# Optimization experiments

Hardware: AMD Instinct MI355X
Metric: run time of the kernel (lower is better)

## Reference

```python
import jax, jax.numpy as jnp
import numpy as np

F_FACETS = 400000
TEX_PER = 4            # textures per facet (counts sum must equal total textures)
T_TEX = F_FACETS * TEX_PER
C_IN = 64
C_OUT = 64
L = 2
N_BASIS = (L + 1) ** 2  # 9
BN_EPS = 1e-3


def setup_inputs() -> dict:
    key = jax.random.key(0)
    k1, k2, k3 = jax.random.split(key, 3)
    input_texture = jax.random.normal(k1, (T_TEX, C_IN), jnp.float32)
    bary_coeff = jax.random.uniform(k2, (T_TEX, N_BASIS), jnp.float32)
    # per-facet texture counts; constant 4 so counts sum exactly to T_TEX
    num_texture = jnp.full((F_FACETS,), TEX_PER, dtype=jnp.int32)
    # xavier_normal_ on [O, I, K]: fan_in = I*K, fan_out = ... torch uses fan_in=I*K? For 3D it treats dim1*rest.
    std = float(np.sqrt(2.0 / (C_IN * N_BASIS + C_OUT * N_BASIS)))
    weights = jax.random.normal(k3, (C_OUT, C_IN, N_BASIS), jnp.float32) * std
    biases = jnp.zeros((1, C_OUT), jnp.float32)
    gamma = jnp.ones((C_OUT,), jnp.float32)
    beta = jnp.zeros((C_OUT,), jnp.float32)
    return {
        "input_texture": input_texture,
        "bary_coeff": bary_coeff,
        "weights": weights,
        "biases": biases,
        "gamma": gamma,
        "beta": beta,
        "num_texture": num_texture,
    }


def reference(input_texture, bary_coeff, weights, biases, gamma, beta, num_texture):
    T = input_texture.shape[0]
    n_facets = num_texture.shape[0]
    n_basis = weights.shape[2]
    # per-texture contribution: contrib[t,o] = sum_{i,k} x[t,i] * W[o,i,k] * bary[t,k]
    # loop over small fixed basis count (9) to avoid a [T, I, K] intermediate
    contrib = jnp.zeros((T, weights.shape[0]), dtype=input_texture.dtype)
    for k in range(n_basis):
        contrib = contrib + (input_texture @ weights[:, :, k].T) * bary_coeff[:, k:k + 1]
    # scatter-sum per facet (ragged groups given by num_texture), then average
    seg_ids = jnp.repeat(jnp.arange(n_facets), num_texture, total_repeat_length=T)
    facet_sum = jax.ops.segment_sum(contrib, seg_ids, num_segments=n_facets)
    out = facet_sum / num_texture[:, None].astype(facet_sum.dtype)
    # bias + ReLU
    out = jax.nn.relu(out + biases)
    # BatchNorm1d in training mode: batch stats (biased variance), eps=1e-3
    mu = jnp.mean(out, axis=0)
    var = jnp.mean(jnp.square(out - mu), axis=0)
    out = (out - mu) * jax.lax.rsqrt(var + BN_EPS) * gamma + beta
    return out
```

## Files before the change

kernel.cpp:

```cpp
#include <hip/hip_runtime.h>


typedef _Float16 half8  __attribute__((ext_vector_type(8)));
typedef _Float16 h2     __attribute__((ext_vector_type(2)));
typedef __fp16   fp16x2 __attribute__((ext_vector_type(2)));
typedef float    f32x4  __attribute__((ext_vector_type(4)));

#define NGROUPS 100000
#define NPAIRS  50000
#define FFACETS 400000
#define GRID1   768
#define LDSP    9472

#define WAITV(N) asm volatile("s_waitcnt vmcnt(" #N ")" ::: "memory")
#define WAITL0() asm volatile("s_waitcnt lgkmcnt(0)" ::: "memory")
#define FENCE()  asm volatile("" ::: "memory")
#define SB0()    __builtin_amdgcn_sched_barrier(0)

union HF { h2 h[4]; half8 v; };

static __device__ __forceinline__ h2 pkrtz(float a, float b) {
    fp16x2 r = __builtin_amdgcn_cvt_pkrtz(a, b);
    return __builtin_bit_cast(h2, r);
}

static __device__ __forceinline__ void gload16(const void* g, void* l) {
    __builtin_amdgcn_global_load_lds((const __attribute__((address_space(1))) void*)g,
                                     (__attribute__((address_space(3))) void*)l, 16, 0, 0);
}

__global__ __launch_bounds__(256) void prep_kernel(const float* __restrict__ W,
                                                   _Float16* __restrict__ wswz,
                                                   float* __restrict__ stats) {
    int idx = blockIdx.x * 256 + threadIdx.x;
    if (idx < 36864) {
        int j    = idx & 7;
        int lane = (idx >> 3) & 63;
        int mt   = (idx >> 9) & 3;
        int c    = idx >> 11;
        int o    = mt * 16 + (lane & 15);
        int i    = (c & 1) * 32 + ((lane >> 4) << 3) + j;
        int kb   = c >> 1;
        wswz[idx] = (_Float16)W[(o * 64 + i) * 9 + kb];
    }
    if (idx < 128) stats[idx] = 0.0f;
}

__global__ __launch_bounds__(256, 3) void pass1_kernel(
    const float* __restrict__ X, const float* __restrict__ BARY,
    const _Float16* __restrict__ WSWZ, const float* __restrict__ BIAS,
    const int* __restrict__ NTEX, float* __restrict__ OUT,
    float* __restrict__ stats) {

    __shared__ __align__(16) char lds[2][LDSP];
    __shared__ float sl_s[64];
    __shared__ float sl_s2[64];

    const int tid  = threadIdx.x;
    const int wave = tid >> 6;
    const int lane = tid & 63;
    const int col  = lane & 15;
    const int quad = lane >> 4;

    half8 wf[18];
#pragma unroll
    for (int c = 0; c < 18; ++c)
        wf[c] = *(const half8*)(WSWZ + ((size_t)(c * 4 + wave) * 64 + lane) * 8);

    const f32x4 biasv = *(const f32x4*)(BIAS + wave * 16 + quad * 4);

    const int pphys  = (wave << 10) + (lane << 4);
    const int xsoff  = pphys ^ (((pphys >> 8) & 7) << 4);
    const char* Xb   = (const char*)X;
    const char* BAb  = (const char*)BARY;
    const char* NTb  = (const char*)NTEX;

    const int m    = (col & 7) << 4;
    const int a00  = (col << 8) + ((quad << 5) ^ m);
    const int a10  = (col << 8) + (((quad << 5) | 16) ^ m);
    const int bco  = 8192 + col * 36;
    const int nco  = 9344 + ((col >> 2) << 2);

    float sacc[4]  = {0.f, 0.f, 0.f, 0.f};
    float s2acc[4] = {0.f, 0.f, 0.f, 0.f};

    const int b = blockIdx.x;
    const int n = (NPAIRS - 1 - b) / GRID1 + 1;

    auto STAGE = [&](int p, int u) {
        const char* xs = Xb + (size_t)u * 8192;
        gload16(xs + xsoff,        &lds[p][pphys]);
        gload16(xs + 4096 + xsoff, &lds[p][4096 + pphys]);
        gload16(BAb + (size_t)u * 1152 + lane * 16, &lds[p][8192 + lane * 16]);
        if (lane < 8) gload16(BAb + (size_t)u * 1152 + 1024 + lane * 16, &lds[p][9216 + lane * 16]);
        if (lane < 2) gload16(NTb + (size_t)u * 32 + lane * 16,          &lds[p][9344 + lane * 16]);
    };

    auto EPI = [&](f32x4 acc, float rc, int f) {
        f32x4 vv;
#pragma unroll
        for (int r = 0; r < 4; ++r) {
            float s = acc[r];
            s += __shfl_xor(s, 1);
            s += __shfl_xor(s, 2);
            s = s * rc + biasv[r];
            s = s > 0.f ? s : 0.f;
            vv[r] = s;
            sacc[r]  += s;
            s2acc[r] += s * s;
        }
        if ((col & 3) == 0)
            *(f32x4*)(OUT + (size_t)f * 64 + wave * 16 + quad * 4) = vv;
    };

    auto ITER = [&](int p, int u, int upre, bool do_stage) {
        __builtin_amdgcn_s_barrier();
        FENCE();
        const char* L = lds[p];
        f32x4 r0[4], r1[4];
        r0[0] = *(const f32x4*)(L + a00);
        r0[1] = *(const f32x4*)(L + a10);
        r0[2] = *(const f32x4*)(L + a00 + 128);
        r0[3] = *(const f32x4*)(L + a10 + 128);
        r1[0] = *(const f32x4*)(L + 4096 + a00);
        r1[1] = *(const f32x4*)(L + 4096 + a10);
        r1[2] = *(const f32x4*)(L + 4096 + a00 + 128);
        r1[3] = *(const f32x4*)(L + 4096 + a10 + 128);
        float bF0[9], bF1[9];
#pragma unroll
        for (int k = 0; k < 9; ++k) bF0[k] = *(const float*)(L + bco + k * 4);
#pragma unroll
        for (int k = 0; k < 9; ++k) bF1[k] = *(const float*)(L + bco + 576 + k * 4);
        const int nt0 = *(const int*)(L + nco);
        const int nt1 = *(const int*)(L + nco + 16);

        h2 xh0[8], xh1[8], bh0[9], bh1[9];
        xh0[0] = pkrtz(r0[0][0], r0[0][1]);  xh0[1] = pkrtz(r0[0][2], r0[0][3]);
        xh0[2] = pkrtz(r0[1][0], r0[1][1]);  xh0[3] = pkrtz(r0[1][2], r0[1][3]);
        xh0[4] = pkrtz(r0[2][0], r0[2][1]);  xh0[5] = pkrtz(r0[2][2], r0[2][3]);
        xh0[6] = pkrtz(r0[3][0], r0[3][1]);  xh0[7] = pkrtz(r0[3][2], r0[3][3]);
        xh1[0] = pkrtz(r1[0][0], r1[0][1]);  xh1[1] = pkrtz(r1[0][2], r1[0][3]);
        xh1[2] = pkrtz(r1[1][0], r1[1][1]);  xh1[3] = pkrtz(r1[1][2], r1[1][3]);
        xh1[4] = pkrtz(r1[2][0], r1[2][1]);  xh1[5] = pkrtz(r1[2][2], r1[2][3]);
        xh1[6] = pkrtz(r1[3][0], r1[3][1]);  xh1[7] = pkrtz(r1[3][2], r1[3][3]);
#pragma unroll
        for (int k = 0; k < 9; ++k) { bh0[k] = pkrtz(bF0[k], bF0[k]); bh1[k] = pkrtz(bF1[k], bF1[k]); }
        const float rc0 = __builtin_amdgcn_rcpf((float)nt0);
        const float rc1 = __builtin_amdgcn_rcpf((float)nt1);

        WAITL0();
        SB0();
        __builtin_amdgcn_s_barrier();
        FENCE();
        if (do_stage) STAGE(p, upre);
        FENCE();

        f32x4 accA = {0.f, 0.f, 0.f, 0.f};
        f32x4 accB = {0.f, 0.f, 0.f, 0.f};
        __builtin_amdgcn_s_setprio(1);
#pragma unroll
        for (int c = 0; c < 18; ++c) {
            const int hh = (c & 1) * 4;
            const h2 bkA = bh0[c >> 1];
            const h2 bkB = bh1[c >> 1];
            HF fa, fb;
            fa.h[0] = xh0[hh + 0] * bkA;  fa.h[1] = xh0[hh + 1] * bkA;
            fa.h[2] = xh0[hh + 2] * bkA;  fa.h[3] = xh0[hh + 3] * bkA;
            accA = __builtin_amdgcn_mfma_f32_16x16x32_f16(wf[c], fa.v, accA, 0, 0, 0);
            fb.h[0] = xh1[hh + 0] * bkB;  fb.h[1] = xh1[hh + 1] * bkB;
            fb.h[2] = xh1[hh + 2] * bkB;  fb.h[3] = xh1[hh + 3] * bkB;
            accB = __builtin_amdgcn_mfma_f32_16x16x32_f16(wf[c], fb.v, accB, 0, 0, 0);
        }
        __builtin_amdgcn_s_setprio(0);

        const int f0 = u * 8 + (col >> 2);
        EPI(accA, rc0, f0);
        EPI(accB, rc1, f0 + 4);
    };

    STAGE(0, b);
    STAGE(1, b + GRID1);
    WAITV(5); ITER(0, b,         b + 2 * GRID1, true);
    WAITV(7); ITER(1, b + GRID1, b + 3 * GRID1, true);
    int t = 2;
    for (; t < n - 2; ++t) {
        WAITV(9);
        ITER(t & 1, b + t * GRID1, b + (t + 2) * GRID1, true);
    }
    WAITV(9); ITER(t & 1, b + t * GRID1, 0, false); ++t;
    WAITV(4); ITER(t & 1, b + t * GRID1, 0, false);

#pragma unroll
    for (int r = 0; r < 4; ++r) {
        float s = sacc[r], s2 = s2acc[r];
        s  += __shfl_xor(s, 1);  s  += __shfl_xor(s, 2);
        s  += __shfl_xor(s, 4);  s  += __shfl_xor(s, 8);
        s2 += __shfl_xor(s2, 1); s2 += __shfl_xor(s2, 2);
        s2 += __shfl_xor(s2, 4); s2 += __shfl_xor(s2, 8);
        if (col == 0) {
            sl_s [wave * 16 + quad * 4 + r] = s  * 0.25f;
            sl_s2[wave * 16 + quad * 4 + r] = s2 * 0.25f;
        }
    }
    __syncthreads();
    if (tid < 64)        atomicAdd(&stats[tid],      sl_s [tid]);
    else if (tid < 128)  atomicAdd(&stats[tid],      sl_s2[tid - 64]);
}

__global__ __launch_bounds__(256) void pass3_kernel(float* __restrict__ OUT,
    const float* __restrict__ stats, const float* __restrict__ gamma,
    const float* __restrict__ beta) {
    const int tid = threadIdx.x;
    const size_t l = (size_t)blockIdx.x * 256 + tid;
    const int c0 = ((int)l & 15) * 4;
    float mu[4], sc[4], be[4];
    const float invF = 1.0f / (float)FFACETS;
#pragma unroll
    for (int u = 0; u < 4; ++u) {
        int ch = c0 + u;
        float m  = stats[ch] * invF;
        float va = stats[64 + ch] * invF - m * m;
        mu[u] = m;
        sc[u] = rsqrtf(va + 1e-3f) * gamma[ch];
        be[u] = beta[ch];
    }
    const size_t n4 = (size_t)FFACETS * 16;
    for (size_t i = l; i < n4; i += (size_t)gridDim.x * 256) {
        f32x4 v = ((f32x4*)OUT)[i];
#pragma unroll
        for (int u = 0; u < 4; ++u)
            v[u] = (v[u] - mu[u]) * sc[u] + be[u];
        ((f32x4*)OUT)[i] = v;
    }
}

extern "C" void kernel_launch(void* const* d_in, const int* in_sizes, int n_in,
                              void* d_out, int out_size, void* d_ws, size_t ws_size,
                              hipStream_t stream) {
    const float* X     = (const float*)d_in[0];
    const float* BARY  = (const float*)d_in[1];
    const float* W     = (const float*)d_in[2];
    const float* BIAS  = (const float*)d_in[3];
    const float* GAMMA = (const float*)d_in[4];
    const float* BETA  = (const float*)d_in[5];
    const int*   NTEX  = (const int*)d_in[6];
    float* OUT = (float*)d_out;

    _Float16* wswz = (_Float16*)d_ws;
    float* stats   = (float*)((char*)d_ws + 73728);

    prep_kernel<<<144, 256, 0, stream>>>(W, wswz, stats);
    pass1_kernel<<<GRID1, 256, 0, stream>>>(X, BARY, wswz, BIAS, NTEX, OUT, stats);
    pass3_kernel<<<2048, 256, 0, stream>>>(OUT, stats, GAMMA, BETA);
}
```

Measured before the change: 674.4 us.

## Fuse BatchNorm pass into main kernel via grid barrier and restructure MFMA basis accumulation

Removes the separate normalization kernel by adding a software grid-wide barrier (atomic counter plus spin) at the end of pass1, after which every block normalizes its own facet pairs in place. The MFMA loop now feeds fp16 inputs directly with separate accumulators per basis, and applies the barycentric weights in fp32 afterwards. This avoids the fp16 multiplies and the extra fp16 rounding of the input, at the cost of more accumulator registers. The grid drops to 512 blocks with occupancy 2 so that all blocks can be co-resident for the barrier, which risks deadlock if they are not.

```diff
diff --git a/kernel.cpp b/kernel.cpp
--- a/kernel.cpp
+++ b/kernel.cpp
@@ -5,11 +5,12 @@
 typedef _Float16 h2     __attribute__((ext_vector_type(2)));
 typedef __fp16   fp16x2 __attribute__((ext_vector_type(2)));
 typedef float    f32x4  __attribute__((ext_vector_type(4)));
+typedef float    f32x2  __attribute__((ext_vector_type(2)));
 
 #define NGROUPS 100000
 #define NPAIRS  50000
 #define FFACETS 400000
-#define GRID1   768
+#define GRID1   512
 #define LDSP    9472
 
 #define WAITV(N) asm volatile("s_waitcnt vmcnt(" #N ")" ::: "memory")
@@ -17,7 +18,7 @@
 #define FENCE()  asm volatile("" ::: "memory")
 #define SB0()    __builtin_amdgcn_sched_barrier(0)
 
-union HF { h2 h[4]; half8 v; };
+union H8 { h2 h[4]; half8 v; };
 
 static __device__ __forceinline__ h2 pkrtz(float a, float b) {
     fp16x2 r = __builtin_amdgcn_cvt_pkrtz(a, b);
@@ -43,14 +44,15 @@
         int kb   = c >> 1;
         wswz[idx] = (_Float16)W[(o * 64 + i) * 9 + kb];
     }
-    if (idx < 128) stats[idx] = 0.0f;
-}
-
-__global__ __launch_bounds__(256, 3) void pass1_kernel(
+    if (idx < 132) stats[idx] = 0.0f;
+}
+
+__global__ __launch_bounds__(256, 2) void pass1_kernel(
     const float* __restrict__ X, const float* __restrict__ BARY,
     const _Float16* __restrict__ WSWZ, const float* __restrict__ BIAS,
     const int* __restrict__ NTEX, float* __restrict__ OUT,
-    float* __restrict__ stats) {
+    float* __restrict__ stats, const float* __restrict__ GAMMA,
+    const float* __restrict__ BETA) {
 
     __shared__ __align__(16) char lds[2][LDSP];
     __shared__ float sl_s[64];
@@ -134,17 +136,15 @@
         const int nt0 = *(const int*)(L + nco);
         const int nt1 = *(const int*)(L + nco + 16);
 
-        h2 xh0[8], xh1[8], bh0[9], bh1[9];
-        xh0[0] = pkrtz(r0[0][0], r0[0][1]);  xh0[1] = pkrtz(r0[0][2], r0[0][3]);
-        xh0[2] = pkrtz(r0[1][0], r0[1][1]);  xh0[3] = pkrtz(r0[1][2], r0[1][3]);
-        xh0[4] = pkrtz(r0[2][0], r0[2][1]);  xh0[5] = pkrtz(r0[2][2], r0[2][3]);
-        xh0[6] = pkrtz(r0[3][0], r0[3][1]);  xh0[7] = pkrtz(r0[3][2], r0[3][3]);
-        xh1[0] = pkrtz(r1[0][0], r1[0][1]);  xh1[1] = pkrtz(r1[0][2], r1[0][3]);
-        xh1[2] = pkrtz(r1[1][0], r1[1][1]);  xh1[3] = pkrtz(r1[1][2], r1[1][3]);
-        xh1[4] = pkrtz(r1[2][0], r1[2][1]);  xh1[5] = pkrtz(r1[2][2], r1[2][3]);
-        xh1[6] = pkrtz(r1[3][0], r1[3][1]);  xh1[7] = pkrtz(r1[3][2], r1[3][3]);
-#pragma unroll
-        for (int k = 0; k < 9; ++k) { bh0[k] = pkrtz(bF0[k], bF0[k]); bh1[k] = pkrtz(bF1[k], bF1[k]); }
+        H8 xlo0, xhi0, xlo1, xhi1;
+        xlo0.h[0] = pkrtz(r0[0][0], r0[0][1]);  xlo0.h[1] = pkrtz(r0[0][2], r0[0][3]);
+        xlo0.h[2] = pkrtz(r0[1][0], r0[1][1]);  xlo0.h[3] = pkrtz(r0[1][2], r0[1][3]);
+        xhi0.h[0] = pkrtz(r0[2][0], r0[2][1]);  xhi0.h[1] = pkrtz(r0[2][2], r0[2][3]);
+        xhi0.h[2] = pkrtz(r0[3][0], r0[3][1]);  xhi0.h[3] = pkrtz(r0[3][2], r0[3][3]);
+        xlo1.h[0] = pkrtz(r1[0][0], r1[0][1]);  xlo1.h[1] = pkrtz(r1[0][2], r1[0][3]);
+        xlo1.h[2] = pkrtz(r1[1][0], r1[1][1]);  xlo1.h[3] = pkrtz(r1[1][2], r1[1][3]);
+        xhi1.h[0] = pkrtz(r1[2][0], r1[2][1]);  xhi1.h[1] = pkrtz(r1[2][2], r1[2][3]);
+        xhi1.h[2] = pkrtz(r1[3][0], r1[3][1]);  xhi1.h[3] = pkrtz(r1[3][2], r1[3][3]);
         const float rc0 = __builtin_amdgcn_rcpf((float)nt0);
         const float rc1 = __builtin_amdgcn_rcpf((float)nt1);
 
@@ -155,24 +155,31 @@
         if (do_stage) STAGE(p, upre);
         FENCE();
 
-        f32x4 accA = {0.f, 0.f, 0.f, 0.f};
-        f32x4 accB = {0.f, 0.f, 0.f, 0.f};
+        f32x4 acc0[9], acc1[9];
+#pragma unroll
+        for (int k = 0; k < 9; ++k) { acc0[k] = (f32x4){0,0,0,0}; acc1[k] = (f32x4){0,0,0,0}; }
         __builtin_amdgcn_s_setprio(1);
 #pragma unroll
-        for (int c = 0; c < 18; ++c) {
-            const int hh = (c & 1) * 4;
-            const h2 bkA = bh0[c >> 1];
-            const h2 bkB = bh1[c >> 1];
-            HF fa, fb;
-            fa.h[0] = xh0[hh + 0] * bkA;  fa.h[1] = xh0[hh + 1] * bkA;
-            fa.h[2] = xh0[hh + 2] * bkA;  fa.h[3] = xh0[hh + 3] * bkA;
-            accA = __builtin_amdgcn_mfma_f32_16x16x32_f16(wf[c], fa.v, accA, 0, 0, 0);
-            fb.h[0] = xh1[hh + 0] * bkB;  fb.h[1] = xh1[hh + 1] * bkB;
-            fb.h[2] = xh1[hh + 2] * bkB;  fb.h[3] = xh1[hh + 3] * bkB;
-            accB = __builtin_amdgcn_mfma_f32_16x16x32_f16(wf[c], fb.v, accB, 0, 0, 0);
+        for (int kb = 0; kb < 9; ++kb) {
+            acc0[kb] = __builtin_amdgcn_mfma_f32_16x16x32_f16(wf[2 * kb],     xlo0.v, acc0[kb], 0, 0, 0);
+            acc1[kb] = __builtin_amdgcn_mfma_f32_16x16x32_f16(wf[2 * kb],     xlo1.v, acc1[kb], 0, 0, 0);
+            acc0[kb] = __builtin_amdgcn_mfma_f32_16x16x32_f16(wf[2 * kb + 1], xhi0.v, acc0[kb], 0, 0, 0);
+            acc1[kb] = __builtin_amdgcn_mfma_f32_16x16x32_f16(wf[2 * kb + 1], xhi1.v, acc1[kb], 0, 0, 0);
         }
         __builtin_amdgcn_s_setprio(0);
 
+        f32x4 accA, accB;
+#pragma unroll
+        for (int r = 0; r < 4; ++r) {
+            float sA = bF0[0] * acc0[0][r];
+            float sB = bF1[0] * acc1[0][r];
+#pragma unroll
+            for (int k = 1; k < 9; ++k) {
+                sA = __builtin_fmaf(bF0[k], acc0[k][r], sA);
+                sB = __builtin_fmaf(bF1[k], acc1[k][r], sB);
+            }
+            accA[r] = sA; accB[r] = sB;
+        }
         const int f0 = u * 8 + (col >> 2);
         EPI(accA, rc0, f0);
         EPI(accB, rc1, f0 + 4);
@@ -205,32 +212,35 @@
     __syncthreads();
     if (tid < 64)        atomicAdd(&stats[tid],      sl_s [tid]);
     else if (tid < 128)  atomicAdd(&stats[tid],      sl_s2[tid - 64]);
-}
-
-__global__ __launch_bounds__(256) void pass3_kernel(float* __restrict__ OUT,
-    const float* __restrict__ stats, const float* __restrict__ gamma,
-    const float* __restrict__ beta) {
-    const int tid = threadIdx.x;
-    const size_t l = (size_t)blockIdx.x * 256 + tid;
-    const int c0 = ((int)l & 15) * 4;
-    float mu[4], sc[4], be[4];
+
+    int* done = (int*)(stats + 128);
+    WAITV(0);
+    __syncthreads();
+    if (tid == 0) {
+        __hip_atomic_fetch_add(done, 1, __ATOMIC_RELEASE, __HIP_MEMORY_SCOPE_AGENT);
+        int spins = 0;
+        while (__hip_atomic_load(done, __ATOMIC_ACQUIRE, __HIP_MEMORY_SCOPE_AGENT) < GRID1
+               && spins < (1 << 30)) { ++spins; __builtin_amdgcn_s_sleep(8); }
+    }
+    __syncthreads();
+
+    const int ch0 = (tid * 2) & 63;
     const float invF = 1.0f / (float)FFACETS;
-#pragma unroll
-    for (int u = 0; u < 4; ++u) {
-        int ch = c0 + u;
-        float m  = stats[ch] * invF;
-        float va = stats[64 + ch] * invF - m * m;
-        mu[u] = m;
-        sc[u] = rsqrtf(va + 1e-3f) * gamma[ch];
-        be[u] = beta[ch];
-    }
-    const size_t n4 = (size_t)FFACETS * 16;
-    for (size_t i = l; i < n4; i += (size_t)gridDim.x * 256) {
-        f32x4 v = ((f32x4*)OUT)[i];
-#pragma unroll
-        for (int u = 0; u < 4; ++u)
-            v[u] = (v[u] - mu[u]) * sc[u] + be[u];
-        ((f32x4*)OUT)[i] = v;
+    float s1a = __hip_atomic_load(&stats[ch0],      __ATOMIC_RELAXED, __HIP_MEMORY_SCOPE_AGENT);
+    float s2a = __hip_atomic_load(&stats[64 + ch0], __ATOMIC_RELAXED, __HIP_MEMORY_SCOPE_AGENT);
+    float s1b = __hip_atomic_load(&stats[ch0 + 1],      __ATOMIC_RELAXED, __HIP_MEMORY_SCOPE_AGENT);
+    float s2b = __hip_atomic_load(&stats[64 + ch0 + 1], __ATOMIC_RELAXED, __HIP_MEMORY_SCOPE_AGENT);
+    float mu0 = s1a * invF, va0 = s2a * invF - mu0 * mu0;
+    float mu1 = s1b * invF, va1 = s2b * invF - mu1 * mu1;
+    float sc0 = rsqrtf(va0 + 1e-3f) * GAMMA[ch0], be0 = BETA[ch0];
+    float sc1 = rsqrtf(va1 + 1e-3f) * GAMMA[ch0 + 1], be1 = BETA[ch0 + 1];
+
+    for (int u = b; u < NPAIRS; u += GRID1) {
+        float* p = OUT + (size_t)u * 512 + tid * 2;
+        f32x2 v = *(f32x2*)p;
+        v[0] = (v[0] - mu0) * sc0 + be0;
+        v[1] = (v[1] - mu1) * sc1 + be1;
+        *(f32x2*)p = v;
     }
 }
 
@@ -250,6 +260,5 @@
     float* stats   = (float*)((char*)d_ws + 73728);
 
     prep_kernel<<<144, 256, 0, stream>>>(W, wswz, stats);
-    pass1_kernel<<<GRID1, 256, 0, stream>>>(X, BARY, wswz, BIAS, NTEX, OUT, stats);
-    pass3_kernel<<<2048, 256, 0, stream>>>(OUT, stats, GAMMA, BETA);
-}
+    pass1_kernel<<<GRID1, 256, 0, stream>>>(X, BARY, wswz, BIAS, NTEX, OUT, stats, GAMMA, BETA);
+}
```

New measurement: 736.6 us. +9.2%, slower.
